# Kernel optimization log

Measured on AMD Instinct MI355X. Metric: run time of the kernel, lower is better.

## Reference

```python
import jax, jax.numpy as jnp
import numpy as np

D_MODEL, N_HEADS = 1024, 16
D_H = D_MODEL // N_HEADS          # 64
D_HR = D_H // 2                   # 32 (decoupled RoPE dim)
D_LATENT = 256
THETA = 10000.0


def rope(x, theta=THETA):
    # x: (..., S, d) with d even; rotate interleaved pairs.
    S, d = x.shape[-2], x.shape[-1]
    inv = theta ** (-jnp.arange(0, d, 2, dtype=jnp.float32) / d)      # (d/2,)
    ang = jnp.arange(S, dtype=jnp.float32)[:, None] * inv             # (S, d/2)
    cos, sin = jnp.cos(ang), jnp.sin(ang)
    x1, x2 = x[..., 0::2], x[..., 1::2]
    r1 = x1 * cos - x2 * sin
    r2 = x1 * sin + x2 * cos
    return jnp.stack([r1, r2], axis=-1).reshape(x.shape)


def setup_inputs() -> dict:
    key = jax.random.key(0)
    ks = jax.random.split(key, 9)
    s = lambda fan_in: 1.0 / np.sqrt(fan_in)
    return {
        "x": jax.random.normal(ks[0], (4, 2048, D_MODEL), jnp.float32),
        "W_DQ": jax.random.normal(ks[1], (D_MODEL, D_LATENT), jnp.float32) * s(D_MODEL),
        "W_UQ": jax.random.normal(ks[2], (D_LATENT, N_HEADS * D_H), jnp.float32) * s(D_LATENT),
        "W_QR": jax.random.normal(ks[3], (D_LATENT, N_HEADS * D_HR), jnp.float32) * s(D_LATENT),
        "W_DKV": jax.random.normal(ks[4], (D_MODEL, D_LATENT), jnp.float32) * s(D_MODEL),
        "W_UK": jax.random.normal(ks[5], (D_LATENT, N_HEADS * D_H), jnp.float32) * s(D_LATENT),
        "W_UV": jax.random.normal(ks[6], (D_LATENT, N_HEADS * D_H), jnp.float32) * s(D_LATENT),
        "W_KR": jax.random.normal(ks[7], (D_MODEL, D_HR), jnp.float32) * s(D_MODEL),
        "W_O": jax.random.normal(ks[8], (N_HEADS * D_H, D_MODEL), jnp.float32) * s(N_HEADS * D_H),
    }


def reference(x, W_DQ, W_UQ, W_QR, W_DKV, W_UK, W_UV, W_KR, W_O):
    B, S, _ = x.shape
    d_qk = D_H + D_HR

    # --- query path: low-rank latent + decoupled RoPE ---
    c_q = x @ W_DQ                                                   # (B,S,L)
    Qc = (c_q @ W_UQ).reshape(B, S, N_HEADS, D_H).transpose(0, 2, 1, 3)   # (B,H,S,dh)
    Qr = (c_q @ W_QR).reshape(B, S, N_HEADS, D_HR).transpose(0, 2, 1, 3)  # (B,H,S,dhr)
    Qr = rope(Qr)

    # --- key/value path: shared latent, shared rotary key ---
    c_kv = x @ W_DKV                                                 # (B,S,L)
    Kc = (c_kv @ W_UK).reshape(B, S, N_HEADS, D_H).transpose(0, 2, 1, 3)  # (B,H,S,dh)
    Kr = rope((x @ W_KR)[:, None, :, :])                             # (B,1,S,dhr)
    Kr = jnp.broadcast_to(Kr, (B, N_HEADS, S, D_HR))
    V = (c_kv @ W_UV).reshape(B, S, N_HEADS, D_H).transpose(0, 2, 1, 3)   # (B,H,S,dh)

    Q = jnp.concatenate([Qc, Qr], axis=-1)                           # (B,H,S,d_qk)
    K = jnp.concatenate([Kc, Kr], axis=-1)

    scores = jnp.einsum('bhqd,bhkd->bhqk', Q, K)
    scores = jnp.clip(scores, -80.0, 80.0)
    causal = jnp.tril(jnp.ones((S, S), dtype=bool))
    scores = jnp.where(causal, scores, -jnp.inf)
    weights = jax.nn.softmax(scores / jnp.sqrt(jnp.float32(d_qk)), axis=-1)
    attn = jnp.einsum('bhqk,bhkd->bhqd', weights, V)                 # (B,H,S,dh)
    attn = attn.transpose(0, 2, 1, 3).reshape(B, S, N_HEADS * D_H)
    return attn @ W_O
```

## Files before the change

kernel.cpp:

```cpp
#include <hip/hip_runtime.h>
#include <hip/hip_bf16.h>


typedef __attribute__((ext_vector_type(8))) __bf16 bf16x8;
typedef __attribute__((ext_vector_type(4))) float f32x4;
typedef __attribute__((ext_vector_type(16))) float f32x16;
typedef __attribute__((ext_vector_type(4))) unsigned short us4;

#define DEV static __device__ __forceinline__

DEV unsigned short f2b(float f) {
  union { __hip_bfloat16 h; unsigned short u; } v;
  v.h = __float2bfloat16(f);
  return v.u;
}
DEV float b2f(unsigned short u) {
  union { unsigned short u; __hip_bfloat16 h; } v;
  v.u = u;
  return __bfloat162float(v.h);
}
DEV unsigned int f2b2(float lo, float hi) {
  union { __hip_bfloat162 h2; unsigned int u; } v;
  float2 t; t.x = lo; t.y = hi;
  v.h2 = __float22bfloat162_rn(t);
  return v.u;
}
DEV f32x4 mfma16(bf16x8 a, bf16x8 b, f32x4 c) {
  return __builtin_amdgcn_mfma_f32_16x16x32_bf16(a, b, c, 0, 0, 0);
}
DEV f32x16 mfma32(bf16x8 a, bf16x8 b, f32x16 c) {
  return __builtin_amdgcn_mfma_f32_32x32x16_bf16(a, b, c, 0, 0, 0);
}
DEV void load_lds16(const void* g, void* lds) {
  __builtin_amdgcn_global_load_lds((__attribute__((address_space(1))) void*)g,
                                   (__attribute__((address_space(3))) void*)lds,
                                   16, 0, 0);
}

__global__ __launch_bounds__(256) void convert_x(const float* __restrict__ x,
                                                 unsigned short* __restrict__ xb) {
  long i = (long)(blockIdx.x * 256 + threadIdx.x) * 4;
  float4 v = *(const float4*)(x + i);
  us4 o = { f2b(v.x), f2b(v.y), f2b(v.z), f2b(v.w) };
  *(us4*)(xb + i) = o;
}

struct TWArgs { const float* W[8]; unsigned short* T[8]; };
__global__ __launch_bounds__(256) void transpose_w_all(TWArgs a) {
  int bid = blockIdx.x;
  int g;
  if      (bid < 256)  g = 0;
  else if (bid < 512)  g = 1;
  else if (bid < 544)  g = 2;
  else if (bid < 800)  g = 3;
  else if (bid < 928)  g = 4;
  else if (bid < 1184) g = 5;
  else if (bid < 1440) g = 6;
  else                 g = 7;
  const int starts[8] = {0, 256, 512, 544, 800, 928, 1184, 1440};
  int local = bid - starts[g];
  int K = (g >= 3 && g <= 6) ? 256 : 1024;
  int N = (g < 2) ? 256 : (g == 2 ? 32 : (g == 4 ? 512 : 1024));
  int tilesX = N >> 5;
  int n0 = (local % tilesX) * 32, k0 = (local / tilesX) * 32;
  const float* W = a.W[g];
  unsigned short* WT = a.T[g];
  __shared__ float tile[32][33];
  int tx = threadIdx.x & 31, ty = threadIdx.x >> 5;
#pragma unroll
  for (int i = 0; i < 32; i += 8)
    tile[ty + i][tx] = W[(size_t)(k0 + ty + i) * N + n0 + tx];
  __syncthreads();
#pragma unroll
  for (int i = 0; i < 32; i += 8)
    WT[(size_t)(n0 + ty + i) * K + k0 + tx] = f2b(tile[tx][ty + i]);
}

__global__ __launch_bounds__(256) void rope_qk(unsigned short* __restrict__ C2,
                                               const unsigned short* __restrict__ C1,
                                               unsigned short* __restrict__ Krr) {
  if (blockIdx.x < 8192) {
    int idx = blockIdx.x * 256 + threadIdx.x;
    int i = idx & 15, h = (idx >> 4) & 15, s = (idx >> 8) & 2047, b = idx >> 19;
    long base = (long)(b * 2048 + s) * 1536 + 1024 + h * 32 + 2 * i;
    float x1 = b2f(C2[base]), x2 = b2f(C2[base + 1]);
    float inv = exp2f(-(float)i * 0.8304820237686285f);
    float ang = (float)s * inv;
    float c = cosf(ang), sn = sinf(ang);
    C2[base]     = f2b(x1 * c - x2 * sn);
    C2[base + 1] = f2b(x1 * sn + x2 * c);
  } else {
    int idx = (blockIdx.x - 8192) * 256 + threadIdx.x;
    int i = idx & 15, s = (idx >> 4) & 2047, b = idx >> 15;
    long src = (long)(b * 2048 + s) * 544 + 512 + 2 * i;
    float x1 = b2f(C1[src]), x2 = b2f(C1[src + 1]);
    float inv = exp2f(-(float)i * 0.8304820237686285f);
    float ang = (float)s * inv;
    float c = cosf(ang), sn = sinf(ang);
    long dst = (long)(b * 2048 + s) * 32 + 2 * i;
    Krr[dst]     = f2b(x1 * c - x2 * sn);
    Krr[dst + 1] = f2b(x1 * sn + x2 * c);
  }
}

template <bool OUT_BF16>
__global__ __launch_bounds__(256) void gemm_bt(const unsigned short* __restrict__ A, int lda,
                                               const unsigned short* __restrict__ Bt, int ldb,
                                               void* __restrict__ Cv, int ldc, int N, int K) {
  __shared__ __align__(16) unsigned short As[128 * 32];
  __shared__ __align__(16) unsigned short Bs[128 * 32];
  const int t = threadIdx.x;
  const int w = t >> 6, lane = t & 63, ln = lane & 15, quad = lane >> 4;
  const int wr = w >> 1, wc = w & 1;
  const int bm0 = blockIdx.x * 128, bn0 = blockIdx.y * 128;
  const int srow = t >> 2;
  const int scol = (t & 3) * 8;
  f32x4 zero = {0.f, 0.f, 0.f, 0.f};
  f32x4 acc[4][4];
#pragma unroll
  for (int i = 0; i < 4; ++i)
#pragma unroll
    for (int j = 0; j < 4; ++j) acc[i][j] = zero;

  for (int k0 = 0; k0 < K; k0 += 32) {
#pragma unroll
    for (int r = 0; r < 2; ++r) {
      int arow = bm0 + r * 64 + srow;
      load_lds16(A + (long)arow * lda + k0 + scol, (char*)As + r * 4096 + w * 1024);
      int brow = bn0 + r * 64 + srow;
      if (brow > N - 1) brow = N - 1;
      load_lds16(Bt + (long)brow * ldb + k0 + scol, (char*)Bs + r * 4096 + w * 1024);
    }
    __syncthreads();
    bf16x8 af[4], bf[4];
#pragma unroll
    for (int i = 0; i < 4; ++i)
      af[i] = *(const bf16x8*)(As + (wr * 64 + i * 16 + ln) * 32 + quad * 8);
#pragma unroll
    for (int j = 0; j < 4; ++j)
      bf[j] = *(const bf16x8*)(Bs + (wc * 64 + j * 16 + ln) * 32 + quad * 8);
#pragma unroll
    for (int i = 0; i < 4; ++i)
#pragma unroll
      for (int j = 0; j < 4; ++j) acc[i][j] = mfma16(af[i], bf[j], acc[i][j]);
    __syncthreads();
  }
#pragma unroll
  for (int i = 0; i < 4; ++i)
#pragma unroll
    for (int j = 0; j < 4; ++j)
#pragma unroll
      for (int r = 0; r < 4; ++r) {
        int row = bm0 + wr * 64 + i * 16 + quad * 4 + r;
        int col = bn0 + wc * 64 + j * 16 + ln;
        if (col < N) {
          if (OUT_BF16)
            ((unsigned short*)Cv)[(long)row * ldc + col] = f2b(acc[i][j][r]);
          else
            ((float*)Cv)[(long)row * ldc + col] = acc[i][j][r];
        }
      }
}

__global__ __launch_bounds__(256) void gemm_bt_vt(const unsigned short* __restrict__ A, int lda,
                                                  const unsigned short* __restrict__ Bt, int ldb,
                                                  unsigned short* __restrict__ Vt, int K) {
  __shared__ __align__(16) unsigned short As[128 * 32];
  __shared__ __align__(16) unsigned short Bs[128 * 32];
  const int t = threadIdx.x;
  const int w = t >> 6, lane = t & 63, ln = lane & 15, quad = lane >> 4;
  const int wr = w >> 1, wc = w & 1;
  const int bm0 = blockIdx.x * 128, bn0 = blockIdx.y * 128;
  const int srow = t >> 2, scol = (t & 3) * 8;
  f32x4 zero = {0.f, 0.f, 0.f, 0.f};
  f32x4 acc[4][4];
#pragma unroll
  for (int i = 0; i < 4; ++i)
#pragma unroll
    for (int j = 0; j < 4; ++j) acc[i][j] = zero;

  for (int k0 = 0; k0 < K; k0 += 32) {
#pragma unroll
    for (int r = 0; r < 2; ++r) {
      load_lds16(A + (long)(bm0 + r * 64 + srow) * lda + k0 + scol, (char*)As + r * 4096 + w * 1024);
      load_lds16(Bt + (long)(bn0 + r * 64 + srow) * ldb + k0 + scol, (char*)Bs + r * 4096 + w * 1024);
    }
    __syncthreads();
    bf16x8 af[4], bf[4];
#pragma unroll
    for (int i = 0; i < 4; ++i)
      af[i] = *(const bf16x8*)(As + (wr * 64 + i * 16 + ln) * 32 + quad * 8);
#pragma unroll
    for (int j = 0; j < 4; ++j)
      bf[j] = *(const bf16x8*)(Bs + (wc * 64 + j * 16 + ln) * 32 + quad * 8);
#pragma unroll
    for (int i = 0; i < 4; ++i)
#pragma unroll
      for (int j = 0; j < 4; ++j) acc[i][j] = mfma16(af[i], bf[j], acc[i][j]);
    __syncthreads();
  }
#pragma unroll
  for (int i = 0; i < 4; ++i)
#pragma unroll
    for (int j = 0; j < 4; ++j) {
      int col = bn0 + wc * 64 + j * 16 + ln;
      int row0 = bm0 + wr * 64 + i * 16 + quad * 4;
      int b = row0 >> 11, sl = row0 & 2047;
      us4 pk = { f2b(acc[i][j][0]), f2b(acc[i][j][1]), f2b(acc[i][j][2]), f2b(acc[i][j][3]) };
      *(us4*)(Vt + ((size_t)(b * 16) * 64 + col) * 2048 + sl) = pk;
    }
}

__global__ __launch_bounds__(256, 4) void flash_attn(const unsigned short* __restrict__ C2,
                                                     const unsigned short* __restrict__ C3,
                                                     const unsigned short* __restrict__ Krr,
                                                     const unsigned short* __restrict__ Vt,
                                                     unsigned short* __restrict__ Oa) {
  __shared__ __align__(16) unsigned short Ks[2][4096];
  __shared__ __align__(16) unsigned short Vs[2][4096];

  const int tid = threadIdx.x;
  const int w = tid >> 6, lane = tid & 63;
  const int l31 = lane & 31, h = lane >> 5;
  const int bh = blockIdx.x, b = bh >> 4, head = bh & 15;
  const int bS = b * 2048;
  const int QPERM[16] = {15, 14, 13, 12, 8, 9, 10, 11, 4, 5, 6, 7, 3, 2, 1, 0};
  const int qi = QPERM[blockIdx.y];
  const int qb = qi * 128 + w * 32;
  const int nkt = 2 * qi + 2;
  const float KSC2  = 0.14724444690f;
  const float KOFF2 = 11.7795557220f;
  const int q = qb + l31;
  const int pr = (l31 & ~12) | ((l31 & 4) << 1) | ((l31 & 8) >> 1);

  const unsigned short* qp = C2 + (size_t)(bS + q) * 1536;
  bf16x8 qf[6];
#pragma unroll
  for (int c = 0; c < 4; ++c)
    qf[c] = *(const bf16x8*)(qp + head * 64 + c * 16 + h * 8);
#pragma unroll
  for (int c = 4; c < 6; ++c)
    qf[c] = *(const bf16x8*)(qp + 1024 + head * 32 + (c - 4) * 16 + h * 8);

  f32x16 o0 = {}, o1 = {};
  float ls0 = 0.f, ls1 = 0.f;

  auto stage = [&](int buf, int key0) {
#pragma unroll
    for (int t = w; t < 8; t += 4) {
      int ci = t * 64 + lane;
      int r = ci >> 3, sl = ci & 7;
      int srcc = sl ^ (r & 7);
      int srck = (r & ~12) | ((r & 4) << 1) | ((r & 8) >> 1);
      load_lds16(C3 + (size_t)(bS + key0 + srck) * 1024 + head * 64 + srcc * 8,
                 &Ks[buf][t * 512]);
    }
#pragma unroll
    for (int t = w; t < 8; t += 4) {
      int ci = t * 64 + lane;
      int r = ci >> 3, sl = ci & 7;
      int srcc = sl ^ (r & 7);
      load_lds16(Vt + (size_t)((size_t)bh * 64 + r) * 2048 + key0 + srcc * 8,
                 &Vs[buf][t * 512]);
    }
  };

  stage(0, 0);
  for (int kt = 0; kt < nkt; ++kt) {
    __syncthreads();
    const int c0 = kt * 64;
    const bool live = (c0 <= qb + 31);
    bf16x8 kr[4];
    if (live) {
#pragma unroll
      for (int m = 0; m < 2; ++m)
#pragma unroll
        for (int c = 0; c < 2; ++c)
          kr[m * 2 + c] = *(const bf16x8*)(Krr + (size_t)(bS + c0 + m * 32 + pr) * 32 +
                                           c * 16 + h * 8);
    }
    if (kt + 1 < nkt) stage((kt + 1) & 1, c0 + 64);
    if (!live) continue;

    const unsigned short* Kp = Ks[kt & 1];
    const unsigned short* Vp = Vs[kt & 1];

#pragma unroll
    for (int m = 0; m < 2; ++m) {
      if (c0 + m * 32 > qb + 31) continue;
      const int r = m * 32 + l31;
      f32x16 s = {};
      __builtin_amdgcn_s_setprio(1);
#pragma unroll
      for (int c = 0; c < 4; ++c) {
        int slot = (2 * c + h) ^ (r & 7);
        bf16x8 kf = *(const bf16x8*)(Kp + r * 64 + slot * 8);
        s = mfma32(kf, qf[c], s);
      }
      s = mfma32(kr[m * 2 + 0], qf[4], s);
      s = mfma32(kr[m * 2 + 1], qf[5], s);
      __builtin_amdgcn_s_setprio(0);

      const bool nm = (c0 + m * 32 + 31) > qb;
      float ev[16];
#pragma unroll
      for (int p = 0; p < 16; ++p) {
        float t = __builtin_amdgcn_fmed3f(s[p], -80.f, 80.f);
        float z = fmaf(t, KSC2, -KOFF2);
        if (nm) {
          int key = c0 + m * 32 + (p & 3) + 4 * ((p >> 2) & 1) + 8 * h + 16 * (p >> 3);
          if (key > q) z = -1e30f;
        }
        float e = exp2f(z);
        if (p & 1) ls1 += e; else ls0 += e;
        ev[p] = e;
      }
      bf16x8 pf[2];
#pragma unroll
      for (int t = 0; t < 2; ++t) {
        union { unsigned int u[4]; bf16x8 v; } pk;
#pragma unroll
        for (int j = 0; j < 4; ++j)
          pk.u[j] = f2b2(ev[t * 8 + 2 * j], ev[t * 8 + 2 * j + 1]);
        pf[t] = pk.v;
      }
      __builtin_amdgcn_s_setprio(1);
#pragma unroll
      for (int t = 0; t < 2; ++t) {
        int tk = m * 2 + t;
#pragma unroll
        for (int n = 0; n < 2; ++n) {
          int rr = n * 32 + l31;
          int slot = (2 * tk + h) ^ (rr & 7);
          bf16x8 vf = *(const bf16x8*)(Vp + rr * 64 + slot * 8);
          if (n == 0) o0 = mfma32(pf[t], vf, o0);
          else        o1 = mfma32(pf[t], vf, o1);
        }
      }
      __builtin_amdgcn_s_setprio(0);
    }
  }

  float lsum = ls0 + ls1;
  float lfull = lsum + __shfl_xor(lsum, 32);
#pragma unroll
  for (int p = 0; p < 16; ++p) {
    int qrow = (p & 3) + 8 * (p >> 2) + 4 * h;
    float rl = 1.0f / __shfl(lfull, qrow);
    size_t base = (size_t)(bS + qb + qrow) * 1024 + head * 64;
    Oa[base + l31]      = f2b(o0[p] * rl);
    Oa[base + 32 + l31] = f2b(o1[p] * rl);
  }
}

extern "C" void kernel_launch(void* const* d_in, const int* in_sizes, int n_in,
                              void* d_out, int out_size, void* d_ws, size_t ws_size,
                              hipStream_t stream) {
  (void)in_sizes; (void)n_in; (void)out_size; (void)ws_size;
  const float* x     = (const float*)d_in[0];
  const float* W_DQ  = (const float*)d_in[1];
  const float* W_UQ  = (const float*)d_in[2];
  const float* W_QR  = (const float*)d_in[3];
  const float* W_DKV = (const float*)d_in[4];
  const float* W_UK  = (const float*)d_in[5];
  const float* W_UV  = (const float*)d_in[6];
  const float* W_KR  = (const float*)d_in[7];
  const float* W_O   = (const float*)d_in[8];

  char* p = (char*)d_ws;
  unsigned short* xb  = (unsigned short*)p; p += (size_t)8192 * 1024 * 2;
  unsigned short* WT1 = (unsigned short*)p; p += (size_t)544 * 1024 * 2;
  unsigned short* WT2 = (unsigned short*)p; p += (size_t)1536 * 256 * 2;
  unsigned short* WT3 = (unsigned short*)p; p += (size_t)2048 * 256 * 2;
  unsigned short* WT4 = (unsigned short*)p; p += (size_t)1024 * 1024 * 2;
  unsigned short* C1  = (unsigned short*)p; p += (size_t)8192 * 544 * 2;
  unsigned short* C2  = (unsigned short*)p; p += (size_t)8192 * 1536 * 2;
  unsigned short* C3  = (unsigned short*)p; p += (size_t)8192 * 1024 * 2;
  unsigned short* Krr = (unsigned short*)p; p += (size_t)8192 * 32 * 2;
  unsigned short* Vt  = (unsigned short*)p; p += (size_t)64 * 64 * 2048 * 2;
  unsigned short* Oa  = (unsigned short*)p; p += (size_t)8192 * 1024 * 2;

  convert_x<<<8192, 256, 0, stream>>>(x, xb);

  TWArgs tw;
  tw.W[0] = W_DQ;  tw.T[0] = WT1;
  tw.W[1] = W_DKV; tw.T[1] = WT1 + 256 * 1024;
  tw.W[2] = W_KR;  tw.T[2] = WT1 + 512 * 1024;
  tw.W[3] = W_UQ;  tw.T[3] = WT2;
  tw.W[4] = W_QR;  tw.T[4] = WT2 + 1024 * 256;
  tw.W[5] = W_UK;  tw.T[5] = WT3;
  tw.W[6] = W_UV;  tw.T[6] = WT3 + 1024 * 256;
  tw.W[7] = W_O;   tw.T[7] = WT4;
  transpose_w_all<<<2464, 256, 0, stream>>>(tw);

  gemm_bt<true><<<dim3(64, 5),  256, 0, stream>>>(xb, 1024, WT1, 1024, C1, 544, 544, 1024);
  gemm_bt<true><<<dim3(64, 12), 256, 0, stream>>>(C1, 544, WT2, 256, C2, 1536, 1536, 256);
  gemm_bt<true><<<dim3(64, 8),  256, 0, stream>>>(C1 + 256, 544, WT3, 256, C3, 1024, 1024, 256);
  gemm_bt_vt<<<dim3(64, 8),     256, 0, stream>>>(C1 + 256, 544, WT3 + 1024 * 256, 256, Vt, 256);
  rope_qk<<<8704, 256, 0, stream>>>(C2, C1, Krr);
  flash_attn<<<dim3(64, 16), 256, 0, stream>>>(C2, C3, Krr, Vt, Oa);
  gemm_bt<false><<<dim3(64, 8), 256, 0, stream>>>(Oa, 1024, WT4, 1024, d_out, 1024, 1024, 1024);
}
```

Before: 298.3 us.

## Split causal attention key range into two halves with a combine kernel

Flash attention now splits each query tile's key range into two halves run as separate blocks. Each block writes unnormalized fp32 partial outputs and row sums, and a new combine kernel sums them and normalizes. The goal is to balance work across the causal triangle and raise block count. Row sums are now computed with an MFMA against a ones vector instead of scalar adds, and the setprio hints are removed. The cost is extra fp32 partial traffic, an extra launch, and a path that depends on workspace size.

```diff
diff --git a/kernel.cpp b/kernel.cpp
--- a/kernel.cpp
+++ b/kernel.cpp
@@ -211,11 +211,14 @@
     }
 }
 
+template <bool SPLIT>
 __global__ __launch_bounds__(256, 4) void flash_attn(const unsigned short* __restrict__ C2,
                                                      const unsigned short* __restrict__ C3,
                                                      const unsigned short* __restrict__ Krr,
                                                      const unsigned short* __restrict__ Vt,
-                                                     unsigned short* __restrict__ Oa) {
+                                                     unsigned short* __restrict__ Oa,
+                                                     float* __restrict__ Po,
+                                                     float* __restrict__ Lp) {
   __shared__ __align__(16) unsigned short Ks[2][4096];
   __shared__ __align__(16) unsigned short Vs[2][4096];
 
@@ -224,10 +227,19 @@
   const int l31 = lane & 31, h = lane >> 5;
   const int bh = blockIdx.x, b = bh >> 4, head = bh & 15;
   const int bS = b * 2048;
-  const int QPERM[16] = {15, 14, 13, 12, 8, 9, 10, 11, 4, 5, 6, 7, 3, 2, 1, 0};
-  const int qi = QPERM[blockIdx.y];
+  int qi, half, kbeg, kend;
+  if (SPLIT) {
+    qi = 15 - (int)(blockIdx.y >> 1);
+    half = blockIdx.y & 1;
+    kbeg = half ? (qi + 1) : 0;
+    kend = half ? (2 * qi + 2) : (qi + 1);
+  } else {
+    qi = 15 - (int)blockIdx.y;
+    half = 0;
+    kbeg = 0;
+    kend = 2 * qi + 2;
+  }
   const int qb = qi * 128 + w * 32;
-  const int nkt = 2 * qi + 2;
   const float KSC2  = 0.14724444690f;
   const float KOFF2 = 11.7795557220f;
   const int q = qb + l31;
@@ -242,8 +254,12 @@
   for (int c = 4; c < 6; ++c)
     qf[c] = *(const bf16x8*)(qp + 1024 + head * 32 + (c - 4) * 16 + h * 8);
 
-  f32x16 o0 = {}, o1 = {};
-  float ls0 = 0.f, ls1 = 0.f;
+  union { unsigned short u[8]; bf16x8 v; } onesu;
+#pragma unroll
+  for (int i = 0; i < 8; ++i) onesu.u[i] = 0x3F80;
+  const bf16x8 ones = onesu.v;
+
+  f32x16 o0 = {}, o1 = {}, osum = {};
 
   auto stage = [&](int buf, int key0) {
 #pragma unroll
@@ -265,8 +281,8 @@
     }
   };
 
-  stage(0, 0);
-  for (int kt = 0; kt < nkt; ++kt) {
+  stage(kbeg & 1, kbeg * 64);
+  for (int kt = kbeg; kt < kend; ++kt) {
     __syncthreads();
     const int c0 = kt * 64;
     const bool live = (c0 <= qb + 31);
@@ -279,7 +295,7 @@
           kr[m * 2 + c] = *(const bf16x8*)(Krr + (size_t)(bS + c0 + m * 32 + pr) * 32 +
                                            c * 16 + h * 8);
     }
-    if (kt + 1 < nkt) stage((kt + 1) & 1, c0 + 64);
+    if (kt + 1 < kend) stage((kt + 1) & 1, (kt + 1) * 64);
     if (!live) continue;
 
     const unsigned short* Kp = Ks[kt & 1];
@@ -290,7 +306,6 @@
       if (c0 + m * 32 > qb + 31) continue;
       const int r = m * 32 + l31;
       f32x16 s = {};
-      __builtin_amdgcn_s_setprio(1);
 #pragma unroll
       for (int c = 0; c < 4; ++c) {
         int slot = (2 * c + h) ^ (r & 7);
@@ -299,7 +314,6 @@
       }
       s = mfma32(kr[m * 2 + 0], qf[4], s);
       s = mfma32(kr[m * 2 + 1], qf[5], s);
-      __builtin_amdgcn_s_setprio(0);
 
       const bool nm = (c0 + m * 32 + 31) > qb;
       float ev[16];
@@ -311,9 +325,7 @@
           int key = c0 + m * 32 + (p & 3) + 4 * ((p >> 2) & 1) + 8 * h + 16 * (p >> 3);
           if (key > q) z = -1e30f;
         }
-        float e = exp2f(z);
-        if (p & 1) ls1 += e; else ls0 += e;
-        ev[p] = e;
+        ev[p] = exp2f(z);
       }
       bf16x8 pf[2];
 #pragma unroll
@@ -324,10 +336,10 @@
           pk.u[j] = f2b2(ev[t * 8 + 2 * j], ev[t * 8 + 2 * j + 1]);
         pf[t] = pk.v;
       }
-      __builtin_amdgcn_s_setprio(1);
 #pragma unroll
       for (int t = 0; t < 2; ++t) {
         int tk = m * 2 + t;
+        osum = mfma32(pf[t], ones, osum);
 #pragma unroll
         for (int n = 0; n < 2; ++n) {
           int rr = n * 32 + l31;
@@ -337,26 +349,55 @@
           else        o1 = mfma32(pf[t], vf, o1);
         }
       }
-      __builtin_amdgcn_s_setprio(0);
-    }
-  }
-
-  float lsum = ls0 + ls1;
-  float lfull = lsum + __shfl_xor(lsum, 32);
-#pragma unroll
-  for (int p = 0; p < 16; ++p) {
-    int qrow = (p & 3) + 8 * (p >> 2) + 4 * h;
-    float rl = 1.0f / __shfl(lfull, qrow);
-    size_t base = (size_t)(bS + qb + qrow) * 1024 + head * 64;
-    Oa[base + l31]      = f2b(o0[p] * rl);
-    Oa[base + 32 + l31] = f2b(o1[p] * rl);
-  }
+    }
+  }
+
+  if (SPLIT) {
+    const int slot = (bh * 16 + qi) * 2 + half;
+    float* po = Po + (size_t)slot * 8192;
+#pragma unroll
+    for (int p = 0; p < 16; ++p) {
+      int qrow = (p & 3) + 8 * (p >> 2) + 4 * h;
+      int rloc = w * 32 + qrow;
+      po[rloc * 64 + l31]      = o0[p];
+      po[rloc * 64 + 32 + l31] = o1[p];
+      if (l31 == 0) Lp[slot * 128 + rloc] = osum[p];
+    }
+  } else {
+#pragma unroll
+    for (int p = 0; p < 16; ++p) {
+      int qrow = (p & 3) + 8 * (p >> 2) + 4 * h;
+      float rl = 1.0f / osum[p];
+      size_t base = (size_t)(bS + qb + qrow) * 1024 + head * 64;
+      Oa[base + l31]      = f2b(o0[p] * rl);
+      Oa[base + 32 + l31] = f2b(o1[p] * rl);
+    }
+  }
+}
+
+__global__ __launch_bounds__(256) void combine_o(const float* __restrict__ Po,
+                                                 const float* __restrict__ Lp,
+                                                 unsigned short* __restrict__ Oa) {
+  int idx = blockIdx.x * 256 + threadIdx.x;
+  int d4 = idx & 15;
+  int r  = (idx >> 4) & 127;
+  int qi = (idx >> 11) & 15;
+  int bh = idx >> 15;
+  int slot = (bh * 16 + qi) * 2;
+  const float4 a = *(const float4*)(Po + ((size_t)slot * 128 + r) * 64 + d4 * 4);
+  const float4 c = *(const float4*)(Po + ((size_t)(slot + 1) * 128 + r) * 64 + d4 * 4);
+  float rl = 1.0f / (Lp[slot * 128 + r] + Lp[(slot + 1) * 128 + r]);
+  int b = bh >> 4, head = bh & 15;
+  size_t orow = (size_t)(b * 2048 + qi * 128 + r);
+  us4 o = { f2b((a.x + c.x) * rl), f2b((a.y + c.y) * rl),
+            f2b((a.z + c.z) * rl), f2b((a.w + c.w) * rl) };
+  *(us4*)(Oa + orow * 1024 + head * 64 + d4 * 4) = o;
 }
 
 extern "C" void kernel_launch(void* const* d_in, const int* in_sizes, int n_in,
                               void* d_out, int out_size, void* d_ws, size_t ws_size,
                               hipStream_t stream) {
-  (void)in_sizes; (void)n_in; (void)out_size; (void)ws_size;
+  (void)in_sizes; (void)n_in; (void)out_size;
   const float* x     = (const float*)d_in[0];
   const float* W_DQ  = (const float*)d_in[1];
   const float* W_UQ  = (const float*)d_in[2];
@@ -379,6 +420,10 @@
   unsigned short* Krr = (unsigned short*)p; p += (size_t)8192 * 32 * 2;
   unsigned short* Vt  = (unsigned short*)p; p += (size_t)64 * 64 * 2048 * 2;
   unsigned short* Oa  = (unsigned short*)p; p += (size_t)8192 * 1024 * 2;
+  float* Po = (float*)p;
+  float* Lp = (float*)(p + (size_t)2048 * 8192 * 4);
+  size_t split_end = ((char*)Lp - (char*)d_ws) + (size_t)2048 * 128 * 4;
+  const bool use_split = ws_size >= split_end;
 
   convert_x<<<8192, 256, 0, stream>>>(x, xb);
 
@@ -398,6 +443,11 @@
   gemm_bt<true><<<dim3(64, 8),  256, 0, stream>>>(C1 + 256, 544, WT3, 256, C3, 1024, 1024, 256);
   gemm_bt_vt<<<dim3(64, 8),     256, 0, stream>>>(C1 + 256, 544, WT3 + 1024 * 256, 256, Vt, 256);
   rope_qk<<<8704, 256, 0, stream>>>(C2, C1, Krr);
-  flash_attn<<<dim3(64, 16), 256, 0, stream>>>(C2, C3, Krr, Vt, Oa);
+  if (use_split) {
+    flash_attn<true><<<dim3(64, 32), 256, 0, stream>>>(C2, C3, Krr, Vt, Oa, Po, Lp);
+    combine_o<<<8192, 256, 0, stream>>>(Po, Lp, Oa);
+  } else {
+    flash_attn<false><<<dim3(64, 16), 256, 0, stream>>>(C2, C3, Krr, Vt, Oa, Po, Lp);
+  }
   gemm_bt<false><<<dim3(64, 8), 256, 0, stream>>>(Oa, 1024, WT4, 1024, d_out, 1024, 1024, 1024);
 }
```

Measured after the change: 363.1 us. 21.7% more time.

## Fold softmax scale into query weights and compute row sums with MFMA

Applied to the files above, without the earlier changes.

Multiplies the W_UQ and W_QR weights by the softmax scale during the bf16 transpose. The attention loop then only clamps scores to the scaled clip bound before exp2, dropping the per-element FMA and offset. Row sums are now accumulated by an extra MFMA against a ones vector instead of VALU adds and end-of-kernel shuffles. The LDS swizzle also XORs in r>>3, the setprio hints are removed, and the query-tile order becomes a simple reverse. The cost is one extra MFMA per P tile. Without the offset, exp values reach about 2^11.8, which fp32 accumulation handles but which changes the bf16 rounding of P.

```diff
diff --git a/kernel.cpp b/kernel.cpp
--- a/kernel.cpp
+++ b/kernel.cpp
@@ -36,6 +36,9 @@
                                    (__attribute__((address_space(3))) void*)lds,
                                    16, 0, 0);
 }
+
+#define KSC2f 0.14724444690f
+#define CLIPf 11.7795557220f
 
 __global__ __launch_bounds__(256) void convert_x(const float* __restrict__ x,
                                                  unsigned short* __restrict__ xb) {
@@ -65,6 +68,7 @@
   int n0 = (local % tilesX) * 32, k0 = (local / tilesX) * 32;
   const float* W = a.W[g];
   unsigned short* WT = a.T[g];
+  float sc = (g == 3 || g == 4) ? KSC2f : 1.0f;
   __shared__ float tile[32][33];
   int tx = threadIdx.x & 31, ty = threadIdx.x >> 5;
 #pragma unroll
@@ -73,7 +77,7 @@
   __syncthreads();
 #pragma unroll
   for (int i = 0; i < 32; i += 8)
-    WT[(size_t)(n0 + ty + i) * K + k0 + tx] = f2b(tile[tx][ty + i]);
+    WT[(size_t)(n0 + ty + i) * K + k0 + tx] = f2b(tile[tx][ty + i] * sc);
 }
 
 __global__ __launch_bounds__(256) void rope_qk(unsigned short* __restrict__ C2,
@@ -224,12 +228,9 @@
   const int l31 = lane & 31, h = lane >> 5;
   const int bh = blockIdx.x, b = bh >> 4, head = bh & 15;
   const int bS = b * 2048;
-  const int QPERM[16] = {15, 14, 13, 12, 8, 9, 10, 11, 4, 5, 6, 7, 3, 2, 1, 0};
-  const int qi = QPERM[blockIdx.y];
+  const int qi = 15 - (int)blockIdx.y;
   const int qb = qi * 128 + w * 32;
   const int nkt = 2 * qi + 2;
-  const float KSC2  = 0.14724444690f;
-  const float KOFF2 = 11.7795557220f;
   const int q = qb + l31;
   const int pr = (l31 & ~12) | ((l31 & 4) << 1) | ((l31 & 8) >> 1);
 
@@ -242,15 +243,19 @@
   for (int c = 4; c < 6; ++c)
     qf[c] = *(const bf16x8*)(qp + 1024 + head * 32 + (c - 4) * 16 + h * 8);
 
-  f32x16 o0 = {}, o1 = {};
-  float ls0 = 0.f, ls1 = 0.f;
+  union { unsigned short u[8]; bf16x8 v; } onesu;
+#pragma unroll
+  for (int i = 0; i < 8; ++i) onesu.u[i] = 0x3F80;
+  const bf16x8 ones = onesu.v;
+
+  f32x16 o0 = {}, o1 = {}, osum = {};
 
   auto stage = [&](int buf, int key0) {
 #pragma unroll
     for (int t = w; t < 8; t += 4) {
       int ci = t * 64 + lane;
       int r = ci >> 3, sl = ci & 7;
-      int srcc = sl ^ (r & 7);
+      int srcc = sl ^ (r & 7) ^ (r >> 3);
       int srck = (r & ~12) | ((r & 4) << 1) | ((r & 8) >> 1);
       load_lds16(C3 + (size_t)(bS + key0 + srck) * 1024 + head * 64 + srcc * 8,
                  &Ks[buf][t * 512]);
@@ -259,7 +264,7 @@
     for (int t = w; t < 8; t += 4) {
       int ci = t * 64 + lane;
       int r = ci >> 3, sl = ci & 7;
-      int srcc = sl ^ (r & 7);
+      int srcc = sl ^ (r & 7) ^ (r >> 3);
       load_lds16(Vt + (size_t)((size_t)bh * 64 + r) * 2048 + key0 + srcc * 8,
                  &Vs[buf][t * 512]);
     }
@@ -290,30 +295,25 @@
       if (c0 + m * 32 > qb + 31) continue;
       const int r = m * 32 + l31;
       f32x16 s = {};
-      __builtin_amdgcn_s_setprio(1);
 #pragma unroll
       for (int c = 0; c < 4; ++c) {
-        int slot = (2 * c + h) ^ (r & 7);
+        int slot = (2 * c + h) ^ (r & 7) ^ (r >> 3);
         bf16x8 kf = *(const bf16x8*)(Kp + r * 64 + slot * 8);
         s = mfma32(kf, qf[c], s);
       }
       s = mfma32(kr[m * 2 + 0], qf[4], s);
       s = mfma32(kr[m * 2 + 1], qf[5], s);
-      __builtin_amdgcn_s_setprio(0);
 
       const bool nm = (c0 + m * 32 + 31) > qb;
       float ev[16];
 #pragma unroll
       for (int p = 0; p < 16; ++p) {
-        float t = __builtin_amdgcn_fmed3f(s[p], -80.f, 80.f);
-        float z = fmaf(t, KSC2, -KOFF2);
+        float z = __builtin_amdgcn_fmed3f(s[p], -CLIPf, CLIPf);
         if (nm) {
           int key = c0 + m * 32 + (p & 3) + 4 * ((p >> 2) & 1) + 8 * h + 16 * (p >> 3);
           if (key > q) z = -1e30f;
         }
-        float e = exp2f(z);
-        if (p & 1) ls1 += e; else ls0 += e;
-        ev[p] = e;
+        ev[p] = exp2f(z);
       }
       bf16x8 pf[2];
 #pragma unroll
@@ -324,29 +324,26 @@
           pk.u[j] = f2b2(ev[t * 8 + 2 * j], ev[t * 8 + 2 * j + 1]);
         pf[t] = pk.v;
       }
-      __builtin_amdgcn_s_setprio(1);
 #pragma unroll
       for (int t = 0; t < 2; ++t) {
         int tk = m * 2 + t;
+        osum = mfma32(pf[t], ones, osum);
 #pragma unroll
         for (int n = 0; n < 2; ++n) {
           int rr = n * 32 + l31;
-          int slot = (2 * tk + h) ^ (rr & 7);
+          int slot = (2 * tk + h) ^ (rr & 7) ^ (rr >> 3);
           bf16x8 vf = *(const bf16x8*)(Vp + rr * 64 + slot * 8);
           if (n == 0) o0 = mfma32(pf[t], vf, o0);
           else        o1 = mfma32(pf[t], vf, o1);
         }
       }
-      __builtin_amdgcn_s_setprio(0);
     }
   }
 
-  float lsum = ls0 + ls1;
-  float lfull = lsum + __shfl_xor(lsum, 32);
 #pragma unroll
   for (int p = 0; p < 16; ++p) {
     int qrow = (p & 3) + 8 * (p >> 2) + 4 * h;
-    float rl = 1.0f / __shfl(lfull, qrow);
+    float rl = 1.0f / osum[p];
     size_t base = (size_t)(bS + qb + qrow) * 1024 + head * 64;
     Oa[base + l31]      = f2b(o0[p] * rl);
     Oa[base + 32 + l31] = f2b(o1[p] * rl);
```

Result: slower. 435.4 us (+46.0%).
